# Kernel optimization log

Measured on AMD Instinct MI355X. Metric: run time of the kernel, lower is better.

The kernel has to match this reference:

```python
import jax, jax.numpy as jnp
import numpy as np

B, S, D = 64, 512, 1024


def setup_inputs() -> dict:
    key = jax.random.key(0)
    k_h, k_w = jax.random.split(key)
    last_hidden_state = jax.random.normal(k_h, (B, S, D), dtype=jnp.float32)
    # word_ids: sorted, contiguous subword->word indices per row (tokenizer word_ids).
    inc = jax.random.bernoulli(k_w, 0.5, (B, S)).astype(jnp.int32)
    inc = inc.at[:, 0].set(0)  # first token starts word 0
    word_ids = jnp.cumsum(inc, axis=1)  # [B, S], max ~ S/2 words
    return {"last_hidden_state": last_hidden_state, "word_ids": word_ids}


def reference(last_hidden_state, word_ids):
    # Faithful, vectorized version of merge_subword_representation:
    # out[i, w] = mean of last_hidden_state[i, t] over t with word_ids[i, t] == w,
    # for w in [0, tot_words_i); remaining positions keep original values.
    b, s, d = last_hidden_state.shape
    seg_sum = jax.vmap(
        lambda h, w: jax.ops.segment_sum(h, w, num_segments=s)
    )(last_hidden_state, word_ids)                                  # [B, S, D]
    cnt = jax.vmap(
        lambda w: jax.ops.segment_sum(jnp.ones((s,), last_hidden_state.dtype), w, num_segments=s)
    )(word_ids)                                                     # [B, S]
    means = seg_sum / jnp.maximum(cnt, 1.0)[..., None]              # safe: valid segments have cnt>=1
    tot_words = jnp.max(word_ids, axis=1) + 1                       # [B]
    pos = jnp.arange(s)
    write_mask = pos[None, :] < tot_words[:, None]                  # [B, S]
    return jnp.where(write_mask[..., None], means, last_hidden_state)
```

## Files before the change

kernel.cpp:

```cpp
#include <hip/hip_runtime.h>

#define BS 64
#define SS 512
#define DD 1024
#define CH 8
#define NCHUNK (SS / CH)
#define QPT 4
#define TASKS (BS * NCHUNK * QPT)
#define NBLOCKS (TASKS / 4)

typedef float f4 __attribute__((ext_vector_type(4)));

__global__ __launch_bounds__(512) void desc_kernel(
    const int* __restrict__ wid,
    unsigned int* __restrict__ desc)
{
    const int b = blockIdx.x;
    const int t = threadIdx.x;
    const int* row = wid + b * SS;

    __shared__ int s_lo[SS + 1];
    __shared__ int s_tot;

    const int w_t  = row[t];
    const int prev = (t == 0) ? -1 : row[t - 1];
    if (t == SS - 1) { s_tot = w_t + 1; s_lo[w_t + 1] = SS; }
    if (w_t != prev) s_lo[w_t] = t;
    __syncthreads();

    unsigned int v = 0;
    if (t >= s_tot) v |= 0x80000000u;
    if (w_t != prev) {
        const int len = s_lo[w_t + 1] - t;
        v |= ((unsigned int)len << 16) | (unsigned int)w_t;
    }
    desc[b * SS + t] = v;
}

__global__ __launch_bounds__(256) void merge_subword_kernel(
    const float* __restrict__ h,
    const unsigned int* __restrict__ desc,
    float* __restrict__ out)
{
    const int wave = (int)threadIdx.x >> 6;
    const int lane = (int)threadIdx.x & 63;
    const int task = (int)blockIdx.x * 4 + wave;

    const int q     = task & 3;
    const int tmp   = task >> 2;
    const int chunk = tmp & (NCHUNK - 1);
    const int b     = tmp >> 6;
    const int t0    = chunk * CH;

    const f4* hp = (const f4*)h;
    f4*       op = (f4*)out;
    const int rowbase = b * SS + t0;
    const int sl      = q * 64 + lane;

    const unsigned int dvec = desc[rowbase + (lane & 7)];

    f4 p[CH];
    #pragma unroll
    for (int i = 0; i < CH; ++i) p[i] = hp[(rowbase + i) * 256 + sl];

    #pragma unroll
    for (int i = 0; i < CH; ++i) {
        const unsigned int d =
            (unsigned int)__builtin_amdgcn_readlane((int)dvec, i);
        if (d & 0x80000000u) {
            op[(rowbase + i) * 256 + sl] = p[i];
        }
        const int len = (int)((d >> 16) & 0x7FFFu);
        if (len) {
            f4 acc = p[i];
            #pragma unroll
            for (int j = 1; j < CH - i; ++j)
                if (j < len) acc += p[i + j];
            for (int j = CH - i; j < len; ++j)
                acc += hp[(rowbase + i + j) * 256 + sl];
            const float inv = 1.0f / (float)len;
            acc *= inv;
            const int w = (int)(d & 0xFFFFu);
            op[(b * SS + w) * 256 + sl] = acc;
        }
    }
}

extern "C" void kernel_launch(void* const* d_in, const int* in_sizes, int n_in,
                              void* d_out, int out_size, void* d_ws, size_t ws_size,
                              hipStream_t stream) {
    (void)in_sizes; (void)n_in; (void)out_size; (void)ws_size;
    const float* h   = (const float*)d_in[0];
    const int*   wid = (const int*)d_in[1];
    float*       out = (float*)d_out;
    unsigned int* desc = (unsigned int*)d_ws;

    desc_kernel<<<dim3(BS), dim3(SS), 0, stream>>>(wid, desc);
    merge_subword_kernel<<<dim3(NBLOCKS), dim3(256), 0, stream>>>(h, desc, out);
}
```

Measured before the change: 53.05 us.

## Process four tasks per wave with double-buffered register prefetch

Each wave now handles four tasks, strided by a quarter of the task space, instead of one, so the grid is a quarter the size. Loads for the next task are issued into a second register buffer before the current task is reduced and stored, so memory latency overlaps with compute. This raises register pressure from the two f4[8] buffers and cuts the number of waves available to hide latency through occupancy.

```diff
diff --git a/kernel.cpp b/kernel.cpp
--- a/kernel.cpp
+++ b/kernel.cpp
@@ -7,7 +7,9 @@
 #define NCHUNK (SS / CH)
 #define QPT 4
 #define TASKS (BS * NCHUNK * QPT)
-#define NBLOCKS (TASKS / 4)
+#define NTASK 4
+#define WAVES_TOTAL (TASKS / NTASK)
+#define NBLOCKS (WAVES_TOTAL / 4)
 
 typedef float f4 __attribute__((ext_vector_type(4)));
 
@@ -44,46 +46,78 @@
 {
     const int wave = (int)threadIdx.x >> 6;
     const int lane = (int)threadIdx.x & 63;
-    const int task = (int)blockIdx.x * 4 + wave;
-
-    const int q     = task & 3;
-    const int tmp   = task >> 2;
-    const int chunk = tmp & (NCHUNK - 1);
-    const int b     = tmp >> 6;
-    const int t0    = chunk * CH;
+    const int wg   = (int)blockIdx.x * 4 + wave;
 
     const f4* hp = (const f4*)h;
     f4*       op = (f4*)out;
-    const int rowbase = b * SS + t0;
-    const int sl      = q * 64 + lane;
 
-    const unsigned int dvec = desc[rowbase + (lane & 7)];
+#define DECODE(task, rb, sl)                                   \
+    {                                                          \
+        const int q_    = (task) & 3;                          \
+        const int tmp_  = (task) >> 2;                         \
+        const int ch_   = tmp_ & (NCHUNK - 1);                 \
+        const int b_    = tmp_ >> 6;                           \
+        rb = b_ * SS + ch_ * CH;                               \
+        sl = q_ * 64 + lane;                                   \
+    }
 
-    f4 p[CH];
-    #pragma unroll
-    for (int i = 0; i < CH; ++i) p[i] = hp[(rowbase + i) * 256 + sl];
+#define ISSUE(p, dv, rb, sl)                                   \
+    {                                                          \
+        dv = desc[(rb) + (lane & 7)];                          \
+        _Pragma("unroll")                                      \
+        for (int i = 0; i < CH; ++i)                           \
+            p[i] = hp[((rb) + i) * 256 + (sl)];                \
+    }
 
-    #pragma unroll
-    for (int i = 0; i < CH; ++i) {
-        const unsigned int d =
-            (unsigned int)__builtin_amdgcn_readlane((int)dvec, i);
-        if (d & 0x80000000u) {
-            op[(rowbase + i) * 256 + sl] = p[i];
-        }
-        const int len = (int)((d >> 16) & 0x7FFFu);
-        if (len) {
-            f4 acc = p[i];
-            #pragma unroll
-            for (int j = 1; j < CH - i; ++j)
-                if (j < len) acc += p[i + j];
-            for (int j = CH - i; j < len; ++j)
-                acc += hp[(rowbase + i + j) * 256 + sl];
-            const float inv = 1.0f / (float)len;
-            acc *= inv;
-            const int w = (int)(d & 0xFFFFu);
-            op[(b * SS + w) * 256 + sl] = acc;
-        }
+#define PROCESS(p, dv, rb, sl)                                            \
+    {                                                                     \
+        const int batch_row0_ = (rb) & ~(SS - 1);                         \
+        _Pragma("unroll")                                                 \
+        for (int i = 0; i < CH; ++i) {                                    \
+            const unsigned int d_ =                                       \
+                (unsigned int)__builtin_amdgcn_readlane((int)(dv), i);    \
+            if (d_ & 0x80000000u) {                                       \
+                op[((rb) + i) * 256 + (sl)] = p[i];                       \
+            }                                                             \
+            const int len_ = (int)((d_ >> 16) & 0x7FFFu);                 \
+            if (len_) {                                                   \
+                f4 acc_ = p[i];                                           \
+                _Pragma("unroll")                                         \
+                for (int j = 1; j < CH - i; ++j)                          \
+                    if (j < len_) acc_ += p[i + j];                       \
+                for (int j = CH - i; j < len_; ++j)                       \
+                    acc_ += hp[((rb) + i + j) * 256 + (sl)];              \
+                acc_ *= (1.0f / (float)len_);                             \
+                const int w_ = (int)(d_ & 0xFFFFu);                       \
+                op[(batch_row0_ + w_) * 256 + (sl)] = acc_;               \
+            }                                                             \
+        }                                                                 \
     }
+
+    f4 pA[CH], pB[CH];
+    unsigned int dA, dB;
+    int rbA, slA, rbB, slB;
+
+    DECODE(wg, rbA, slA);
+    ISSUE(pA, dA, rbA, slA);
+
+    DECODE(wg + WAVES_TOTAL, rbB, slB);
+    ISSUE(pB, dB, rbB, slB);
+    PROCESS(pA, dA, rbA, slA);
+
+    DECODE(wg + 2 * WAVES_TOTAL, rbA, slA);
+    ISSUE(pA, dA, rbA, slA);
+    PROCESS(pB, dB, rbB, slB);
+
+    DECODE(wg + 3 * WAVES_TOTAL, rbB, slB);
+    ISSUE(pB, dB, rbB, slB);
+    PROCESS(pA, dA, rbA, slA);
+
+    PROCESS(pB, dB, rbB, slB);
+
+#undef DECODE
+#undef ISSUE
+#undef PROCESS
 }
 
 extern "C" void kernel_launch(void* const* d_in, const int* in_sizes, int n_in,
```

After: 52.71 us. Within noise of the previous version (-0.6%).

## Fuse segment descriptor computation into merge kernel via wave ballot

Applied to the files above, without the earlier changes.

Removes the separate descriptor kernel and computes word boundaries inside each wave by loading word_ids for the chunk plus lookahead, using shfl_up and ballot to find segment starts and lengths. This eliminates one kernel launch and the workspace round trip between the two kernels. Segments longer than the 64-lane window fall back to a serial scan over word_ids. The cost is redundant word_id loads per wave and extra scalar bit work.

```diff
diff --git a/kernel.cpp b/kernel.cpp
--- a/kernel.cpp
+++ b/kernel.cpp
@@ -11,36 +11,10 @@
 
 typedef float f4 __attribute__((ext_vector_type(4)));
 
-__global__ __launch_bounds__(512) void desc_kernel(
-    const int* __restrict__ wid,
-    unsigned int* __restrict__ desc)
-{
-    const int b = blockIdx.x;
-    const int t = threadIdx.x;
-    const int* row = wid + b * SS;
-
-    __shared__ int s_lo[SS + 1];
-    __shared__ int s_tot;
-
-    const int w_t  = row[t];
-    const int prev = (t == 0) ? -1 : row[t - 1];
-    if (t == SS - 1) { s_tot = w_t + 1; s_lo[w_t + 1] = SS; }
-    if (w_t != prev) s_lo[w_t] = t;
-    __syncthreads();
-
-    unsigned int v = 0;
-    if (t >= s_tot) v |= 0x80000000u;
-    if (w_t != prev) {
-        const int len = s_lo[w_t + 1] - t;
-        v |= ((unsigned int)len << 16) | (unsigned int)w_t;
-    }
-    desc[b * SS + t] = v;
-}
-
 __global__ __launch_bounds__(256) void merge_subword_kernel(
     const float* __restrict__ h,
-    const unsigned int* __restrict__ desc,
-    float* __restrict__ out)
+    const int*   __restrict__ wid,
+    float*       __restrict__ out)
 {
     const int wave = (int)threadIdx.x >> 6;
     const int lane = (int)threadIdx.x & 63;
@@ -54,34 +28,54 @@
 
     const f4* hp = (const f4*)h;
     f4*       op = (f4*)out;
-    const int rowbase = b * SS + t0;
-    const int sl      = q * 64 + lane;
+    const int browbase = b * SS;
+    const int rowbase  = browbase + t0;
+    const int sl       = q * 64 + lane;
 
-    const unsigned int dvec = desc[rowbase + (lane & 7)];
+    const int idx = t0 + lane;
+    int v = (idx < SS) ? wid[browbase + idx] : -(2 + lane);
+
+    const int wprev = (t0 == 0) ? -1 : wid[browbase + t0 - 1];
+    const int tot   = wid[browbase + SS - 1] + 1;
 
     f4 p[CH];
     #pragma unroll
     for (int i = 0; i < CH; ++i) p[i] = hp[(rowbase + i) * 256 + sl];
 
+    int vp = __shfl_up(v, 1);
+    const bool changed = (lane == 0) ? (v != wprev) : (v != vp);
+    const unsigned long long M = __ballot(changed);
+
     #pragma unroll
     for (int i = 0; i < CH; ++i) {
-        const unsigned int d =
-            (unsigned int)__builtin_amdgcn_readlane((int)dvec, i);
-        if (d & 0x80000000u) {
+        if (t0 + i >= tot) {
             op[(rowbase + i) * 256 + sl] = p[i];
         }
-        const int len = (int)((d >> 16) & 0x7FFFu);
-        if (len) {
+        if ((M >> i) & 1ull) {
+            const int w = __builtin_amdgcn_readlane(v, i);
+            const unsigned long long rest = M >> (i + 1);
+            const int len = rest ? __ffsll((unsigned long long)rest) : 0;
             f4 acc = p[i];
-            #pragma unroll
-            for (int j = 1; j < CH - i; ++j)
-                if (j < len) acc += p[i + j];
-            for (int j = CH - i; j < len; ++j)
-                acc += hp[(rowbase + i + j) * 256 + sl];
-            const float inv = 1.0f / (float)len;
-            acc *= inv;
-            const int w = (int)(d & 0xFFFFu);
-            op[(b * SS + w) * 256 + sl] = acc;
+            if (len) {
+                #pragma unroll
+                for (int j = 1; j < CH - i; ++j)
+                    if (j < len) acc += p[i + j];
+                for (int j = CH - i; j < len; ++j)
+                    acc += hp[(rowbase + i + j) * 256 + sl];
+                acc *= (1.0f / (float)len);
+                op[(browbase + w) * 256 + sl] = acc;
+            } else {
+                #pragma unroll
+                for (int j = 1; j < CH - i; ++j) acc += p[i + j];
+                int cnt = CH - i;
+                int tt = t0 + CH;
+                while (tt < SS && wid[browbase + tt] == w) {
+                    acc += hp[(browbase + tt) * 256 + sl];
+                    ++cnt; ++tt;
+                }
+                acc *= (1.0f / (float)cnt);
+                op[(browbase + w) * 256 + sl] = acc;
+            }
         }
     }
 }
@@ -89,12 +83,10 @@
 extern "C" void kernel_launch(void* const* d_in, const int* in_sizes, int n_in,
                               void* d_out, int out_size, void* d_ws, size_t ws_size,
                               hipStream_t stream) {
-    (void)in_sizes; (void)n_in; (void)out_size; (void)ws_size;
+    (void)in_sizes; (void)n_in; (void)out_size; (void)d_ws; (void)ws_size;
     const float* h   = (const float*)d_in[0];
     const int*   wid = (const int*)d_in[1];
     float*       out = (float*)d_out;
-    unsigned int* desc = (unsigned int*)d_ws;
 
-    desc_kernel<<<dim3(BS), dim3(SS), 0, stream>>>(wid, desc);
-    merge_subword_kernel<<<dim3(NBLOCKS), dim3(256), 0, stream>>>(h, desc, out);
+    merge_subword_kernel<<<dim3(NBLOCKS), dim3(256), 0, stream>>>(h, wid, out);
 }
```

New measurement: 48.55 us. -8.5%, faster.
